# Kernel tuning notes

Hardware: AMD Instinct MI355X
Metric: run time of the kernel (lower is better)

Reference implementation:

```python
import jax, jax.numpy as jnp
import numpy as np

N, E, G = 50000, 800000, 512
HD, ED, GD, HID = 128, 64, 64, 128  # h_dim, e_dim, g_dim, hid_dim


def _mlp2(x, W1, b1, W2, b2, last_act):
    # Linear -> ReLU -> Linear (-> optional last activation)
    y = jax.nn.relu(x @ W1 + b1) @ W2 + b2
    return last_act(y) if last_act is not None else y


def setup_inputs() -> dict:
    key = jax.random.key(0)
    ks = list(jax.random.split(key, 24))
    ki = iter(ks)

    def p(shape):
        return (jax.random.normal(next(ki), shape, jnp.float32) * 0.02)

    inp = {
        "h": jax.random.normal(next(ki), (N, HD), jnp.float32),
        "e_index": jax.random.randint(next(ki), (2, E), 0, N),
        "e": jax.random.normal(next(ki), (E, ED), jnp.float32),
        "g": jax.random.normal(next(ki), (G, GD), jnp.float32),
        "batch": jnp.sort(jax.random.randint(next(ki), (N,), 0, G)),
        # fc_m: [2*HD+ED+GD, HID, HID], last_activation=relu
        "W_m1": p((2 * HD + ED + GD, HID)), "b_m1": jnp.zeros((HID,), jnp.float32),
        "W_m2": p((HID, HID)), "b_m2": jnp.zeros((HID,), jnp.float32),
        # fc_m_att: [HID, 1], sigmoid
        "W_ma": p((HID, 1)), "b_ma": jnp.zeros((1,), jnp.float32),
        # fc_e: [HID, ED, ED]
        "W_e1": p((HID, ED)), "b_e1": jnp.zeros((ED,), jnp.float32),
        "W_e2": p((ED, ED)), "b_e2": jnp.zeros((ED,), jnp.float32),
        # fc_h: [HD+HID+GD, HD, HD]
        "W_h1": p((HD + HID + GD, HD)), "b_h1": jnp.zeros((HD,), jnp.float32),
        "W_h2": p((HD, HD)), "b_h2": jnp.zeros((HD,), jnp.float32),
        # fc_h_att: [HD, 1]
        "W_ha": p((HD, 1)), "b_ha": jnp.zeros((1,), jnp.float32),
        # fc_g: [GD+HD, GD, GD]
        "W_g1": p((GD + HD, GD)), "b_g1": jnp.zeros((GD,), jnp.float32),
        "W_g2": p((GD, GD)), "b_g2": jnp.zeros((GD,), jnp.float32),
    }
    return inp


def reference(h, e_index, e, g, batch,
              W_m1, b_m1, W_m2, b_m2, W_ma, b_ma,
              W_e1, b_e1, W_e2, b_e2,
              W_h1, b_h1, W_h2, b_h2, W_ha, b_ha,
              W_g1, b_g1, W_g2, b_g2):
    src, dst = e_index[0], e_index[1]
    e_batch = batch[dst]

    # edge message: concat gathered endpoints + edge feat + gathered global
    m_cat = jnp.concatenate([h[src], h[dst], e, g[e_batch]], axis=1)  # [E, 2HD+ED+GD]
    m = jax.nn.relu(jax.nn.relu(m_cat @ W_m1 + b_m1) @ W_m2 + b_m2)   # [E, HID]
    m_att = jax.nn.sigmoid(m @ W_ma + b_ma)                            # [E, 1]

    e_update = _mlp2(m, W_e1, b_e1, W_e2, b_e2, None)                  # [E, ED]
    e_out = jax.nn.relu(e + e_update)

    m_aggr = jax.ops.segment_sum(m_att * m, dst, num_segments=h.shape[0])  # [N, HID]

    h_cat = jnp.concatenate([h, m_aggr, g[batch]], axis=1)             # [N, HD+HID+GD]
    h_update = _mlp2(h_cat, W_h1, b_h1, W_h2, b_h2, None)
    h_out = jax.nn.relu(h + h_update)                                  # [N, HD]
    h_att = h_out @ W_ha + b_ha                                        # [N, 1]

    h_aggr = jax.ops.segment_sum(h_att * h_out, batch, num_segments=g.shape[0])  # [G, HD]

    g_cat = jnp.concatenate([g, h_aggr], axis=1)                       # [G, GD+HD]
    g_update = _mlp2(g_cat, W_g1, b_g1, W_g2, b_g2, None)
    g_out = jax.nn.relu(g + g_update)

    return (h_out, e_out, g_out)
```

## Files before the change

kernel.cpp:

```cpp
#include <hip/hip_runtime.h>
#include <hip/hip_bf16.h>

#define NN 50000
#define NE 800000
#define NG 512
#define HD 128
#define ED 64
#define GD 64
#define HID 128
#define EB 64

typedef __attribute__((ext_vector_type(8))) short short8;
typedef __attribute__((ext_vector_type(4))) short short4v;
typedef __attribute__((ext_vector_type(2))) float f32x2;
typedef __attribute__((ext_vector_type(4))) float f32x4;

__device__ __forceinline__ short f2bf(float f) {
  union { float f; unsigned u; } v; v.f = f;
  unsigned r = v.u + 0x7fffu + ((v.u >> 16) & 1u);
  return (short)(r >> 16);
}

__device__ __forceinline__ float bf2f(short s) {
  union { unsigned u; float f; } v;
  v.u = ((unsigned)(unsigned short)s) << 16;
  return v.f;
}

__device__ __forceinline__ short8 load_a8(const float* p) {
  const f32x4* q = (const f32x4*)p;
  f32x4 x0 = q[0], x1 = q[1];
  short8 r;
  r[0]=f2bf(x0[0]); r[1]=f2bf(x0[1]); r[2]=f2bf(x0[2]); r[3]=f2bf(x0[3]);
  r[4]=f2bf(x1[0]); r[5]=f2bf(x1[1]); r[6]=f2bf(x1[2]); r[7]=f2bf(x1[3]);
  return r;
}

__device__ __forceinline__ int swz(int row, int col, int rowBytes) {
  int b = row * rowBytes + col * 2;
  b ^= (row & 7) << 4;
  return b >> 1;
}

__global__ void pack_kernel(const float* __restrict__ Wm1, const float* __restrict__ Wm2,
                            const float* __restrict__ We1, const float* __restrict__ We2,
                            const float* __restrict__ Wh1, const float* __restrict__ Wh2,
                            short* __restrict__ out) {
  int gid = blockIdx.x * 256 + threadIdx.x;
  if (gid >= 135168) return;
  const float* W; int Ncol, base, idx;
  if (gid < 49152)       { W = Wm1; Ncol = 128; base = 0;      idx = gid; }
  else if (gid < 65536)  { W = Wm2; Ncol = 128; base = 49152;  idx = gid - 49152; }
  else if (gid < 73728)  { W = We1; Ncol = 64;  base = 65536;  idx = gid - 65536; }
  else if (gid < 77824)  { W = We2; Ncol = 64;  base = 73728;  idx = gid - 73728; }
  else if (gid < 118784) { W = Wh1; Ncol = 128; base = 77824;  idx = gid - 77824; }
  else                   { W = Wh2; Ncol = 128; base = 118784; idx = gid - 118784; }
  int k = idx / Ncol, n = idx % Ncol;
  out[base + (k >> 3) * Ncol * 8 + n * 8 + (k & 7)] = f2bf(W[idx]);
}

__global__ void cast_kernel(const float* __restrict__ h, const float* __restrict__ g,
                            const float* __restrict__ e, const int* __restrict__ ei,
                            short* __restrict__ h_bf, short* __restrict__ g_bf,
                            short* __restrict__ e_bf, int* __restrict__ deg) {
  int gid = blockIdx.x * 256 + threadIdx.x;
  const int H4 = NN * HD / 4;
  const int G4 = NG * GD / 4;
  const int E4 = NE * ED / 4;
  if (gid < H4) {
    f32x4 v = ((const f32x4*)h)[gid];
    short4v r; r[0]=f2bf(v[0]); r[1]=f2bf(v[1]); r[2]=f2bf(v[2]); r[3]=f2bf(v[3]);
    *(short4v*)(h_bf + gid * 4) = r;
  } else if (gid < H4 + G4) {
    int i = gid - H4;
    f32x4 v = ((const f32x4*)g)[i];
    short4v r; r[0]=f2bf(v[0]); r[1]=f2bf(v[1]); r[2]=f2bf(v[2]); r[3]=f2bf(v[3]);
    *(short4v*)(g_bf + i * 4) = r;
  } else if (gid < H4 + G4 + E4) {
    int i = gid - H4 - G4;
    f32x4 v = ((const f32x4*)e)[i];
    short4v r; r[0]=f2bf(v[0]); r[1]=f2bf(v[1]); r[2]=f2bf(v[2]); r[3]=f2bf(v[3]);
    *(short4v*)(e_bf + i * 4) = r;
  } else if (gid < H4 + G4 + E4 + NE) {
    int i = gid - H4 - G4 - E4;
    atomicAdd(&deg[ei[NE + i]], 1);
  }
}

__global__ __launch_bounds__(1024) void scan_kernel(int* __restrict__ deg) {
  __shared__ int psum[1024];
  const int CH = 49;
  int t = threadIdx.x;
  int lo = t * CH, hi = lo + CH; if (hi > NN) hi = NN; if (lo > NN) lo = NN;
  int s = 0;
  for (int i = lo; i < hi; ++i) s += deg[i];
  psum[t] = s;
  __syncthreads();
  for (int d = 1; d < 1024; d <<= 1) {
    int v = (t >= d) ? psum[t - d] : 0;
    __syncthreads();
    psum[t] += v;
    __syncthreads();
  }
  int run = (t == 0) ? 0 : psum[t - 1];
  for (int i = lo; i < hi; ++i) { int v = deg[i]; deg[i] = run; run += v; }
}

__global__ void scatter_kernel(const int* __restrict__ ei, int* __restrict__ off,
                               int* __restrict__ elist) {
  int i = blockIdx.x * 256 + threadIdx.x;
  if (i < NE) {
    int d = ei[NE + i];
    int p = atomicAdd(&off[d], 1);
    elist[p] = i;
  }
}

__global__ __launch_bounds__(256) void edge_kernel(
    const short* __restrict__ h_bf, const int* __restrict__ ei,
    const short* __restrict__ e_bf, const short* __restrict__ g_bf,
    const int* __restrict__ batch, const int* __restrict__ elist,
    const short* __restrict__ pWm1, const float* __restrict__ bm1,
    const short* __restrict__ pWm2, const float* __restrict__ bm2,
    const float* __restrict__ Wma, const float* __restrict__ bma,
    const short* __restrict__ pWe1, const float* __restrict__ be1,
    const short* __restrict__ pWe2, const float* __restrict__ be2,
    float* __restrict__ e_out, float* __restrict__ m_aggr) {
  __shared__ short lds_m[EB * 128];
  __shared__ short bufB[2][4096];
  __shared__ float att_s[EB];
  __shared__ int sdst[EB];
  __shared__ int seid[EB];
  short* ebuf = lds_m;

  const int tid = threadIdx.x;
  const int w = tid >> 6;
  const int lane = tid & 63;
  const int row16 = lane & 15;
  const int quad = lane >> 4;
  const int eb = blockIdx.x * EB;

#define STAGE(Wp, c, b) do {                                                  \
    const short* _s = (Wp) + (size_t)(c) * 4096;                              \
    short8 _v0 = *(const short8*)(_s + tid * 8);                              \
    short8 _v1 = *(const short8*)(_s + 2048 + tid * 8);                       \
    *(short8*)&bufB[(b)][tid * 8] = _v0;                                      \
    *(short8*)&bufB[(b)][2048 + tid * 8] = _v1;                               \
  } while (0)

  if (tid < EB) {
    int eid = elist[eb + tid];
    seid[tid] = eid;
    sdst[tid] = ei[NE + eid];
  }

  const int eidr = elist[eb + w * 16 + row16];
  const int dstr = ei[NE + eidr];
  const int srcr = ei[eidr];
  const int gbr = batch[dstr];

  const short* seg0 = h_bf + (size_t)srcr * HD;
  const short* seg1 = h_bf + (size_t)dstr * HD;
  const short* seg2 = e_bf + (size_t)eidr * ED;
  const short* seg3 = g_bf + (size_t)gbr * GD;

  f32x4 acc[8];
#pragma unroll
  for (int t = 0; t < 8; ++t) acc[t] = (f32x4)0.0f;

  STAGE(pWm1, 0, 0);
  __syncthreads();
#pragma unroll
  for (int c = 0; c < 12; ++c) {
    if (c < 11) STAGE(pWm1, c + 1, (c + 1) & 1);
    else        STAGE(pWm2, 0, 0);
    const short* src; int off;
    if (c < 4)       { src = seg0; off = c * 32; }
    else if (c < 8)  { src = seg1; off = (c - 4) * 32; }
    else if (c < 10) { src = seg2; off = (c - 8) * 32; }
    else             { src = seg3; off = (c - 10) * 32; }
    short8 a = *(const short8*)(src + off + quad * 8);
    const short* bc = &bufB[c & 1][quad * 1024 + row16 * 8];
#pragma unroll
    for (int t = 0; t < 8; ++t) {
      short8 b = *(const short8*)(bc + t * 128);
      acc[t] = __builtin_amdgcn_mfma_f32_16x16x32_bf16(a, b, acc[t], 0, 0, 0);
    }
    __syncthreads();
  }
#pragma unroll
  for (int t = 0; t < 8; ++t) {
    float b1 = bm1[t * 16 + row16];
#pragma unroll
    for (int r = 0; r < 4; ++r) {
      float y = fmaxf(acc[t][r] + b1, 0.f);
      lds_m[swz(w * 16 + quad * 4 + r, t * 16 + row16, 256)] = f2bf(y);
    }
  }

  f32x4 acc2[8];
#pragma unroll
  for (int t = 0; t < 8; ++t) acc2[t] = (f32x4)0.0f;
#pragma unroll
  for (int c = 0; c < 4; ++c) {
    if (c < 3) STAGE(pWm2, c + 1, (c + 1) & 1);
    short8 a = *(const short8*)&lds_m[swz(w * 16 + row16, c * 32 + quad * 8, 256)];
    const short* bc = &bufB[c & 1][quad * 1024 + row16 * 8];
#pragma unroll
    for (int t = 0; t < 8; ++t) {
      short8 b = *(const short8*)(bc + t * 128);
      acc2[t] = __builtin_amdgcn_mfma_f32_16x16x32_bf16(a, b, acc2[t], 0, 0, 0);
    }
    __syncthreads();
  }

  float p[4] = {0.f, 0.f, 0.f, 0.f};
#pragma unroll
  for (int t = 0; t < 8; ++t) {
    float b2 = bm2[t * 16 + row16];
    float wv = Wma[t * 16 + row16];
#pragma unroll
    for (int r = 0; r < 4; ++r) {
      float y = fmaxf(acc2[t][r] + b2, 0.f);
      lds_m[swz(w * 16 + quad * 4 + r, t * 16 + row16, 256)] = f2bf(y);
      p[r] += y * wv;
    }
  }

#pragma unroll
  for (int s = 1; s < 16; s <<= 1) {
#pragma unroll
    for (int r = 0; r < 4; ++r) p[r] += __shfl_xor(p[r], s, 64);
  }
  {
    float bma0 = bma[0];
    if (row16 == 0) {
#pragma unroll
      for (int r = 0; r < 4; ++r)
        att_s[w * 16 + quad * 4 + r] = 1.f / (1.f + __expf(-(p[r] + bma0)));
    }
  }

  f32x4 acc3[4];
#pragma unroll
  for (int t = 0; t < 4; ++t) acc3[t] = (f32x4)0.0f;
#pragma unroll
  for (int c = 0; c < 4; ++c) {
    short8 a = *(const short8*)&lds_m[swz(w * 16 + row16, c * 32 + quad * 8, 256)];
    const short* bp = pWe1 + (size_t)(c * 4 + quad) * (ED * 8) + row16 * 8;
#pragma unroll
    for (int t = 0; t < 4; ++t) {
      short8 b = *(const short8*)(bp + t * 16 * 8);
      acc3[t] = __builtin_amdgcn_mfma_f32_16x16x32_bf16(a, b, acc3[t], 0, 0, 0);
    }
  }

  __syncthreads();

  {
    int cp = tid & 63;
    int r0 = (tid >> 6) * 16;
    int cur = sdst[r0];
    float s0 = 0.f, s1 = 0.f;
    bool first = true;
#pragma unroll 1
    for (int r = r0; r < r0 + 16; ++r) {
      int d = sdst[r];
      unsigned u = *(const unsigned*)&lds_m[swz(r, cp * 2, 256)];
      float av = att_s[r];
      float v0 = bf2f((short)(u & 0xffffu)) * av;
      float v1 = bf2f((short)(u >> 16)) * av;
      if (d != cur) {
        if (first) {
          atomicAdd(&m_aggr[(size_t)cur * HID + cp * 2], s0);
          atomicAdd(&m_aggr[(size_t)cur * HID + cp * 2 + 1], s1);
        } else {
          f32x2 st; st[0] = s0; st[1] = s1;
          *(f32x2*)&m_aggr[(size_t)cur * HID + cp * 2] = st;
        }
        first = false; cur = d; s0 = v0; s1 = v1;
      } else {
        s0 += v0; s1 += v1;
      }
    }
    atomicAdd(&m_aggr[(size_t)cur * HID + cp * 2], s0);
    atomicAdd(&m_aggr[(size_t)cur * HID + cp * 2 + 1], s1);
  }

  __syncthreads();

#pragma unroll
  for (int t = 0; t < 4; ++t) {
    float b1 = be1[t * 16 + row16];
#pragma unroll
    for (int r = 0; r < 4; ++r) {
      float y = fmaxf(acc3[t][r] + b1, 0.f);
      ebuf[swz(w * 16 + quad * 4 + r, t * 16 + row16, 128)] = f2bf(y);
    }
  }

  f32x4 acc4[4];
#pragma unroll
  for (int t = 0; t < 4; ++t) acc4[t] = (f32x4)0.0f;
#pragma unroll
  for (int c = 0; c < 2; ++c) {
    short8 a = *(const short8*)&ebuf[swz(w * 16 + row16, c * 32 + quad * 8, 128)];
    const short* bp = pWe2 + (size_t)(c * 4 + quad) * (ED * 8) + row16 * 8;
#pragma unroll
    for (int t = 0; t < 4; ++t) {
      short8 b = *(const short8*)(bp + t * 16 * 8);
      acc4[t] = __builtin_amdgcn_mfma_f32_16x16x32_bf16(a, b, acc4[t], 0, 0, 0);
    }
  }

  int eidS[4];
#pragma unroll
  for (int r = 0; r < 4; ++r) eidS[r] = seid[w * 16 + quad * 4 + r];
#pragma unroll
  for (int t = 0; t < 4; ++t) {
    float b2 = be2[t * 16 + row16];
#pragma unroll
    for (int r = 0; r < 4; ++r) {
      int col = t * 16 + row16;
      float res = bf2f(e_bf[(size_t)eidS[r] * ED + col]);
      float v = res + acc4[t][r] + b2;
      e_out[(size_t)eidS[r] * ED + col] = fmaxf(v, 0.f);
    }
  }
#undef STAGE
}

__global__ __launch_bounds__(256) void node_kernel(
    const float* __restrict__ h, const short* __restrict__ h_bf,
    const float* __restrict__ m_aggr, const short* __restrict__ g_bf,
    const int* __restrict__ batch,
    const short* __restrict__ pWh1, const float* __restrict__ bh1,
    const short* __restrict__ pWh2, const float* __restrict__ bh2,
    const float* __restrict__ Wha, const float* __restrict__ bha,
    float* __restrict__ h_out, float* __restrict__ h_aggr) {
  __shared__ short lds_y[4][16 * 128];
  __shared__ int sbat[64];

  const int wave = threadIdx.x >> 6;
  const int lane = threadIdx.x & 63;
  const int row16 = lane & 15;
  const int quad = lane >> 4;
  const int nbase = blockIdx.x * 64 + wave * 16;

  int nA = nbase + row16;
  int nAc = nA < NN ? nA : NN - 1;
  int gbA = batch[nAc];
  if (quad == 0) sbat[wave * 16 + row16] = (nA < NN) ? gbA : -1;

  short8 afr[10];
  {
    const short* s0 = h_bf + (size_t)nAc * HD;
    const float* s1 = m_aggr + (size_t)nAc * HID;
    const short* s2 = g_bf + (size_t)gbA * GD;
#pragma unroll
    for (int c = 0; c < 4; ++c) afr[c] = *(const short8*)(s0 + c * 32 + quad * 8);
#pragma unroll
    for (int c = 0; c < 4; ++c) afr[4 + c] = load_a8(s1 + c * 32 + quad * 8);
    afr[8] = *(const short8*)(s2 + quad * 8);
    afr[9] = *(const short8*)(s2 + 32 + quad * 8);
  }

  f32x4 acc[8];
#pragma unroll
  for (int t = 0; t < 8; ++t) acc[t] = (f32x4)0.0f;
#pragma unroll
  for (int c = 0; c < 10; ++c) {
    const short* bp = pWh1 + (size_t)(c * 4 + quad) * HD * 8 + row16 * 8;
#pragma unroll
    for (int t = 0; t < 8; ++t) {
      short8 b = *(const short8*)(bp + t * 16 * 8);
      acc[t] = __builtin_amdgcn_mfma_f32_16x16x32_bf16(afr[c], b, acc[t], 0, 0, 0);
    }
  }
#pragma unroll
  for (int t = 0; t < 8; ++t) {
    float b1 = bh1[t * 16 + row16];
#pragma unroll
    for (int r = 0; r < 4; ++r) {
      float y = fmaxf(acc[t][r] + b1, 0.f);
      lds_y[wave][swz(quad * 4 + r, t * 16 + row16, 256)] = f2bf(y);
    }
  }

  f32x4 acc2[8];
#pragma unroll
  for (int t = 0; t < 8; ++t) acc2[t] = (f32x4)0.0f;
#pragma unroll
  for (int c = 0; c < 4; ++c) {
    short8 a = *(const short8*)&lds_y[wave][swz(row16, c * 32 + quad * 8, 256)];
    const short* bp = pWh2 + (size_t)(c * 4 + quad) * HD * 8 + row16 * 8;
#pragma unroll
    for (int t = 0; t < 8; ++t) {
      short8 b = *(const short8*)(bp + t * 16 * 8);
      acc2[t] = __builtin_amdgcn_mfma_f32_16x16x32_bf16(a, b, acc2[t], 0, 0, 0);
    }
  }

  float hval[8][4];
  int nS[4];
#pragma unroll
  for (int r = 0; r < 4; ++r) nS[r] = nbase + quad * 4 + r;
#pragma unroll
  for (int t = 0; t < 8; ++t) {
    float b2 = bh2[t * 16 + row16];
#pragma unroll
    for (int r = 0; r < 4; ++r) {
      float v = 0.f;
      if (nS[r] < NN) {
        v = h[(size_t)nS[r] * HD + t * 16 + row16] + acc2[t][r] + b2;
        v = fmaxf(v, 0.f);
        h_out[(size_t)nS[r] * HD + t * 16 + row16] = v;
      }
      hval[t][r] = v;
    }
  }

  float part[4] = {0.f, 0.f, 0.f, 0.f};
#pragma unroll
  for (int t = 0; t < 8; ++t) {
    float w = Wha[t * 16 + row16];
#pragma unroll
    for (int r = 0; r < 4; ++r) part[r] += hval[t][r] * w;
  }
#pragma unroll
  for (int s = 1; s < 16; s <<= 1) {
#pragma unroll
    for (int r = 0; r < 4; ++r) part[r] += __shfl_xor(part[r], s, 64);
  }
  float bha0 = bha[0];
#pragma unroll
  for (int t = 0; t < 8; ++t)
#pragma unroll
    for (int r = 0; r < 4; ++r)
      lds_y[wave][swz(quad * 4 + r, t * 16 + row16, 256)] =
          f2bf((part[r] + bha0) * hval[t][r]);

  __syncthreads();

  {
    int col = threadIdx.x & 127;
    int r0 = (threadIdx.x >> 7) * 32;
    int cur = sbat[r0];
    float sum = 0.f;
    bool first = true;
#pragma unroll 1
    for (int r = r0; r < r0 + 32; ++r) {
      int d = sbat[r];
      float v = bf2f(lds_y[r >> 4][swz(r & 15, col, 256)]);
      if (d != cur) {
        if (cur >= 0) {
          if (first) atomicAdd(&h_aggr[(size_t)cur * HD + col], sum);
          else h_aggr[(size_t)cur * HD + col] = sum;
        }
        first = false; cur = d; sum = v;
      } else {
        sum += v;
      }
    }
    if (cur >= 0) atomicAdd(&h_aggr[(size_t)cur * HD + col], sum);
  }
}

__global__ void g_kernel(const float* __restrict__ g, const float* __restrict__ h_aggr,
                         const float* __restrict__ Wg1, const float* __restrict__ bg1,
                         const float* __restrict__ Wg2, const float* __restrict__ bg2,
                         float* __restrict__ g_out) {
  __shared__ float cat[192];
  __shared__ float y1[64];
  int r = blockIdx.x;
  int t = threadIdx.x;
  cat[t] = g[(size_t)r * GD + t];
  cat[64 + t] = h_aggr[(size_t)r * HD + t];
  cat[128 + t] = h_aggr[(size_t)r * HD + 64 + t];
  __syncthreads();
  float a = bg1[t];
  for (int k = 0; k < 192; ++k) a += cat[k] * Wg1[k * 64 + t];
  y1[t] = fmaxf(a, 0.f);
  __syncthreads();
  float b = bg2[t];
  for (int k = 0; k < 64; ++k) b += y1[k] * Wg2[k * 64 + t];
  float v = g[(size_t)r * GD + t] + b;
  g_out[(size_t)r * GD + t] = fmaxf(v, 0.f);
}

extern "C" void kernel_launch(void* const* d_in, const int* in_sizes, int n_in,
                              void* d_out, int out_size, void* d_ws, size_t ws_size,
                              hipStream_t stream) {
  const float* h = (const float*)d_in[0];
  const int* ei = (const int*)d_in[1];
  const float* e = (const float*)d_in[2];
  const float* g = (const float*)d_in[3];
  const int* batch = (const int*)d_in[4];
  const float* Wm1 = (const float*)d_in[5];
  const float* bm1 = (const float*)d_in[6];
  const float* Wm2 = (const float*)d_in[7];
  const float* bm2 = (const float*)d_in[8];
  const float* Wma = (const float*)d_in[9];
  const float* bma = (const float*)d_in[10];
  const float* We1 = (const float*)d_in[11];
  const float* be1 = (const float*)d_in[12];
  const float* We2 = (const float*)d_in[13];
  const float* be2 = (const float*)d_in[14];
  const float* Wh1 = (const float*)d_in[15];
  const float* bh1 = (const float*)d_in[16];
  const float* Wh2 = (const float*)d_in[17];
  const float* bh2 = (const float*)d_in[18];
  const float* Wha = (const float*)d_in[19];
  const float* bha = (const float*)d_in[20];
  const float* Wg1 = (const float*)d_in[21];
  const float* bg1 = (const float*)d_in[22];
  const float* Wg2 = (const float*)d_in[23];
  const float* bg2 = (const float*)d_in[24];

  float* out = (float*)d_out;
  float* h_out = out;
  float* e_out = out + (size_t)NN * HD;
  float* g_out = e_out + (size_t)NE * ED;

  char* ws = (char*)d_ws;
  float* m_aggr = (float*)ws;
  float* h_aggr = (float*)(ws + 25600000);
  short* packed = (short*)(ws + 25862144);
  int* deg      = (int*)(ws + 26132480);
  int* elist    = (int*)(ws + 26332480);
  short* h_bf   = (short*)(ws + 29532480);
  short* g_bf   = (short*)(ws + 42332480);
  short* e_bf   = (short*)(ws + 42398016);
  short* pWm1 = packed;
  short* pWm2 = packed + 49152;
  short* pWe1 = packed + 65536;
  short* pWe2 = packed + 73728;
  short* pWh1 = packed + 77824;
  short* pWh2 = packed + 118784;

  hipMemsetAsync(m_aggr, 0, (size_t)NN * HID * 4, stream);
  hipMemsetAsync(h_aggr, 0, (size_t)NG * HD * 4, stream);
  hipMemsetAsync(deg, 0, (size_t)NN * 4, stream);

  pack_kernel<<<(135168 + 255) / 256, 256, 0, stream>>>(Wm1, Wm2, We1, We2, Wh1, Wh2, packed);
  cast_kernel<<<(15208192 + 255) / 256, 256, 0, stream>>>(h, g, e, ei, h_bf, g_bf, e_bf, deg);
  scan_kernel<<<1, 1024, 0, stream>>>(deg);
  scatter_kernel<<<(NE + 255) / 256, 256, 0, stream>>>(ei, deg, elist);

  edge_kernel<<<NE / EB, 256, 0, stream>>>(h_bf, ei, e_bf, g_bf, batch, elist,
                                           pWm1, bm1, pWm2, bm2, Wma, bma,
                                           pWe1, be1, pWe2, be2, e_out, m_aggr);

  node_kernel<<<(NN + 63) / 64, 256, 0, stream>>>(h, h_bf, m_aggr, g_bf, batch,
                                                  pWh1, bh1, pWh2, bh2, Wha, bha,
                                                  h_out, h_aggr);

  g_kernel<<<NG, 64, 0, stream>>>(g, h_aggr, Wg1, bg1, Wg2, bg2, g_out);
}
```

Baseline: 659.9 us.

## Read fp32 edge features directly in edge kernel, remap blocks per XCD, raise MFMA priority

Removes the separate fp32-to-bf16 cast pass over the edge feature tensor; the edge kernel now loads fp32 e and converts it to bf16 inline for the first GEMM, and uses fp32 e for the residual. This removes a full read and write pass over e but doubles the bytes the edge kernel reads for e. It also remaps block indices so each XCD processes a contiguous range of edges for better L2 locality, and raises wave priority around MFMA loops.

Measured after the change: 631.9 us. -4.3%, faster.

```diff
diff --git a/kernel.cpp b/kernel.cpp
--- a/kernel.cpp
+++ b/kernel.cpp
@@ -60,13 +60,12 @@
 }
 
 __global__ void cast_kernel(const float* __restrict__ h, const float* __restrict__ g,
-                            const float* __restrict__ e, const int* __restrict__ ei,
+                            const int* __restrict__ ei,
                             short* __restrict__ h_bf, short* __restrict__ g_bf,
-                            short* __restrict__ e_bf, int* __restrict__ deg) {
+                            int* __restrict__ deg) {
   int gid = blockIdx.x * 256 + threadIdx.x;
   const int H4 = NN * HD / 4;
   const int G4 = NG * GD / 4;
-  const int E4 = NE * ED / 4;
   if (gid < H4) {
     f32x4 v = ((const f32x4*)h)[gid];
     short4v r; r[0]=f2bf(v[0]); r[1]=f2bf(v[1]); r[2]=f2bf(v[2]); r[3]=f2bf(v[3]);
@@ -76,13 +75,8 @@
     f32x4 v = ((const f32x4*)g)[i];
     short4v r; r[0]=f2bf(v[0]); r[1]=f2bf(v[1]); r[2]=f2bf(v[2]); r[3]=f2bf(v[3]);
     *(short4v*)(g_bf + i * 4) = r;
-  } else if (gid < H4 + G4 + E4) {
+  } else if (gid < H4 + G4 + NE) {
     int i = gid - H4 - G4;
-    f32x4 v = ((const f32x4*)e)[i];
-    short4v r; r[0]=f2bf(v[0]); r[1]=f2bf(v[1]); r[2]=f2bf(v[2]); r[3]=f2bf(v[3]);
-    *(short4v*)(e_bf + i * 4) = r;
-  } else if (gid < H4 + G4 + E4 + NE) {
-    int i = gid - H4 - G4 - E4;
     atomicAdd(&deg[ei[NE + i]], 1);
   }
 }
@@ -118,7 +112,7 @@
 
 __global__ __launch_bounds__(256) void edge_kernel(
     const short* __restrict__ h_bf, const int* __restrict__ ei,
-    const short* __restrict__ e_bf, const short* __restrict__ g_bf,
+    const float* __restrict__ e, const short* __restrict__ g_bf,
     const int* __restrict__ batch, const int* __restrict__ elist,
     const short* __restrict__ pWm1, const float* __restrict__ bm1,
     const short* __restrict__ pWm2, const float* __restrict__ bm2,
@@ -138,7 +132,13 @@
   const int lane = tid & 63;
   const int row16 = lane & 15;
   const int quad = lane >> 4;
-  const int eb = blockIdx.x * EB;
+
+  int nwg = gridDim.x;
+  int q = nwg >> 3, rr = nwg & 7;
+  int xcd = blockIdx.x & 7;
+  int idx = blockIdx.x >> 3;
+  int bid = (xcd < rr ? xcd * (q + 1) : rr * (q + 1) + (xcd - rr) * q) + idx;
+  const int eb = bid * EB;
 
 #define STAGE(Wp, c, b) do {                                                  \
     const short* _s = (Wp) + (size_t)(c) * 4096;                              \
@@ -161,7 +161,7 @@
 
   const short* seg0 = h_bf + (size_t)srcr * HD;
   const short* seg1 = h_bf + (size_t)dstr * HD;
-  const short* seg2 = e_bf + (size_t)eidr * ED;
+  const float* seg2 = e + (size_t)eidr * ED;
   const short* seg3 = g_bf + (size_t)gbr * GD;
 
   f32x4 acc[8];
@@ -174,18 +174,19 @@
   for (int c = 0; c < 12; ++c) {
     if (c < 11) STAGE(pWm1, c + 1, (c + 1) & 1);
     else        STAGE(pWm2, 0, 0);
-    const short* src; int off;
-    if (c < 4)       { src = seg0; off = c * 32; }
-    else if (c < 8)  { src = seg1; off = (c - 4) * 32; }
-    else if (c < 10) { src = seg2; off = (c - 8) * 32; }
-    else             { src = seg3; off = (c - 10) * 32; }
-    short8 a = *(const short8*)(src + off + quad * 8);
+    short8 a;
+    if (c < 4)       a = *(const short8*)(seg0 + c * 32 + quad * 8);
+    else if (c < 8)  a = *(const short8*)(seg1 + (c - 4) * 32 + quad * 8);
+    else if (c < 10) a = load_a8(seg2 + (c - 8) * 32 + quad * 8);
+    else             a = *(const short8*)(seg3 + (c - 10) * 32 + quad * 8);
     const short* bc = &bufB[c & 1][quad * 1024 + row16 * 8];
+    __builtin_amdgcn_s_setprio(1);
 #pragma unroll
     for (int t = 0; t < 8; ++t) {
       short8 b = *(const short8*)(bc + t * 128);
       acc[t] = __builtin_amdgcn_mfma_f32_16x16x32_bf16(a, b, acc[t], 0, 0, 0);
     }
+    __builtin_amdgcn_s_setprio(0);
     __syncthreads();
   }
 #pragma unroll
@@ -206,11 +207,13 @@
     if (c < 3) STAGE(pWm2, c + 1, (c + 1) & 1);
     short8 a = *(const short8*)&lds_m[swz(w * 16 + row16, c * 32 + quad * 8, 256)];
     const short* bc = &bufB[c & 1][quad * 1024 + row16 * 8];
+    __builtin_amdgcn_s_setprio(1);
 #pragma unroll
     for (int t = 0; t < 8; ++t) {
       short8 b = *(const short8*)(bc + t * 128);
       acc2[t] = __builtin_amdgcn_mfma_f32_16x16x32_bf16(a, b, acc2[t], 0, 0, 0);
     }
+    __builtin_amdgcn_s_setprio(0);
     __syncthreads();
   }
 
@@ -248,11 +251,13 @@
   for (int c = 0; c < 4; ++c) {
     short8 a = *(const short8*)&lds_m[swz(w * 16 + row16, c * 32 + quad * 8, 256)];
     const short* bp = pWe1 + (size_t)(c * 4 + quad) * (ED * 8) + row16 * 8;
+    __builtin_amdgcn_s_setprio(1);
 #pragma unroll
     for (int t = 0; t < 4; ++t) {
       short8 b = *(const short8*)(bp + t * 16 * 8);
       acc3[t] = __builtin_amdgcn_mfma_f32_16x16x32_bf16(a, b, acc3[t], 0, 0, 0);
     }
+    __builtin_amdgcn_s_setprio(0);
   }
 
   __syncthreads();
@@ -306,11 +311,13 @@
   for (int c = 0; c < 2; ++c) {
     short8 a = *(const short8*)&ebuf[swz(w * 16 + row16, c * 32 + quad * 8, 128)];
     const short* bp = pWe2 + (size_t)(c * 4 + quad) * (ED * 8) + row16 * 8;
+    __builtin_amdgcn_s_setprio(1);
 #pragma unroll
     for (int t = 0; t < 4; ++t) {
       short8 b = *(const short8*)(bp + t * 16 * 8);
       acc4[t] = __builtin_amdgcn_mfma_f32_16x16x32_bf16(a, b, acc4[t], 0, 0, 0);
     }
+    __builtin_amdgcn_s_setprio(0);
   }
 
   int eidS[4];
@@ -322,7 +329,7 @@
 #pragma unroll
     for (int r = 0; r < 4; ++r) {
       int col = t * 16 + row16;
-      float res = bf2f(e_bf[(size_t)eidS[r] * ED + col]);
+      float res = e[(size_t)eidS[r] * ED + col];
       float v = res + acc4[t][r] + b2;
       e_out[(size_t)eidS[r] * ED + col] = fmaxf(v, 0.f);
     }
@@ -530,7 +537,6 @@
   int* elist    = (int*)(ws + 26332480);
   short* h_bf   = (short*)(ws + 29532480);
   short* g_bf   = (short*)(ws + 42332480);
-  short* e_bf   = (short*)(ws + 42398016);
   short* pWm1 = packed;
   short* pWm2 = packed + 49152;
   short* pWe1 = packed + 65536;
@@ -543,11 +549,11 @@
   hipMemsetAsync(deg, 0, (size_t)NN * 4, stream);
 
   pack_kernel<<<(135168 + 255) / 256, 256, 0, stream>>>(Wm1, Wm2, We1, We2, Wh1, Wh2, packed);
-  cast_kernel<<<(15208192 + 255) / 256, 256, 0, stream>>>(h, g, e, ei, h_bf, g_bf, e_bf, deg);
+  cast_kernel<<<(2408192 + 255) / 256, 256, 0, stream>>>(h, g, ei, h_bf, g_bf, deg);
   scan_kernel<<<1, 1024, 0, stream>>>(deg);
   scatter_kernel<<<(NE + 255) / 256, 256, 0, stream>>>(ei, deg, elist);
 
-  edge_kernel<<<NE / EB, 256, 0, stream>>>(h_bf, ei, e_bf, g_bf, batch, elist,
+  edge_kernel<<<NE / EB, 256, 0, stream>>>(h_bf, ei, e, g_bf, batch, elist,
                                            pWm1, bm1, pWm2, bm2, Wma, bma,
                                            pWe1, be1, pWe2, be2, e_out, m_aggr);
 
```
